# Kernel tuning notes

Measured on AMD Instinct MI355X. Metric: run time of the kernel, lower is better.

The kernel has to match this reference:

```python
import jax, jax.numpy as jnp
import numpy as np

NUM_HEADS = 16
EMB = 1024
HEAD = 64
SEQ = 2048
BATCH = 4


def setup_inputs() -> dict:
    key = jax.random.key(0)
    ks = jax.random.split(key, 6)
    s = EMB ** -0.5
    x = jax.random.normal(ks[0], (BATCH, SEQ, EMB), dtype=jnp.float32)
    # per-head projection weights stacked: [H, E, D] (Linear(emb, head, bias=False) per head)
    Wq = jax.random.normal(ks[1], (NUM_HEADS, EMB, HEAD), dtype=jnp.float32) * s
    Wk = jax.random.normal(ks[2], (NUM_HEADS, EMB, HEAD), dtype=jnp.float32) * s
    Wv = jax.random.normal(ks[3], (NUM_HEADS, EMB, HEAD), dtype=jnp.float32) * s
    # output projection Linear(head*num_heads, emb): weight [E, H*D], bias [E]
    Wo = jax.random.normal(ks[4], (EMB, NUM_HEADS * HEAD), dtype=jnp.float32) * ((NUM_HEADS * HEAD) ** -0.5)
    bo = jax.random.normal(ks[5], (EMB,), dtype=jnp.float32) * 0.01
    return {"x": x, "Wq": Wq, "Wk": Wk, "Wv": Wv, "Wo": Wo, "bo": bo}


def reference(x, Wq, Wk, Wv, Wo, bo):
    B, S, E = x.shape
    scale = HEAD ** -0.5
    # batched per-head projections: [B, H, S, D]
    q = jnp.einsum('bse,hed->bhsd', x, Wq)
    k = jnp.einsum('bse,hed->bhsd', x, Wk)
    v = jnp.einsum('bse,hed->bhsd', x, Wv)
    scores = jnp.einsum('bhqd,bhkd->bhqk', q, k) * scale
    causal = jnp.tril(jnp.ones((S, S), dtype=bool))
    scores = jnp.where(causal, scores, jnp.finfo(scores.dtype).min)
    attn = jax.nn.softmax(scores, axis=-1)  # dropout disabled (eval/deterministic)
    ctx = jnp.einsum('bhqk,bhkd->bhqd', attn, v)
    # concat heads along last dim (head-major order, matching torch.cat)
    concat = ctx.transpose(0, 2, 1, 3).reshape(B, S, NUM_HEADS * HEAD)
    out = concat @ Wo.T + bo
    return out
```

## Files before the change

### kernel.cpp

```cpp
#include <hip/hip_runtime.h>

#define NHEADS 16
#define EMB 1024
#define HDIM 64
#define SEQ 2048
#define BATCH 4

typedef unsigned short u16;
typedef __attribute__((ext_vector_type(8))) __bf16 bf16x8;
typedef __attribute__((ext_vector_type(4))) float f32x4;

#if __has_builtin(__builtin_amdgcn_exp2f)
#define EXP2(x) __builtin_amdgcn_exp2f(x)
#else
#define EXP2(x) __expf((x)*0.69314718056f)
#endif
#define CL2E 0.18033688011112042f

#define BARRIER() __builtin_amdgcn_s_barrier()
#define SB0() __builtin_amdgcn_sched_barrier(0)
#define PRIO1() __builtin_amdgcn_s_setprio(1)
#define PRIO0() __builtin_amdgcn_s_setprio(0)
#define VMCNT(n) asm volatile("s_waitcnt vmcnt(" #n ")" ::: "memory")
#define LGKM0() asm volatile("s_waitcnt lgkmcnt(0)" ::: "memory")

__device__ __forceinline__ u16 f2bf(float f) {
  union { float f; unsigned u; } v; v.f = f;
  unsigned r = v.u + 0x7fffu + ((v.u >> 16) & 1u);
  return (u16)(r >> 16);
}
__device__ __forceinline__ unsigned pk2bf(float a, float b) {
  union { __bf16 h[2]; unsigned u; } x;
  x.h[0] = (__bf16)a; x.h[1] = (__bf16)b; return x.u;
}
__device__ __forceinline__ void gl16(const void* g, void* l) {
  __builtin_amdgcn_global_load_lds(
      (const __attribute__((address_space(1))) unsigned*)g,
      (__attribute__((address_space(3))) unsigned*)l, 16, 0, 0);
}
__device__ __forceinline__ unsigned PKLO(unsigned a, unsigned b) {
  return __builtin_amdgcn_perm(a, b, 0x01000504u);
}
__device__ __forceinline__ unsigned PKHI(unsigned a, unsigned b) {
  return __builtin_amdgcn_perm(a, b, 0x03020706u);
}

__global__ __launch_bounds__(256) void k_prep(const float* __restrict__ x,
                                              const float* __restrict__ Wo,
                                              const float* __restrict__ Wq,
                                              const float* __restrict__ Wk,
                                              const float* __restrict__ Wv,
                                              u16* __restrict__ Xb,
                                              u16* __restrict__ Wob,
                                              u16* __restrict__ Wt) {
  __shared__ u16 sT[64][65];
  const int bid = blockIdx.x;
  const int t = threadIdx.x;
  if (bid < 8192) {
    int i = bid * 256 + t;
    f32x4 v = *(const f32x4*)(x + (size_t)i * 4);
    uint2 o;
    o.x = (unsigned)f2bf(v[0]) | ((unsigned)f2bf(v[1]) << 16);
    o.y = (unsigned)f2bf(v[2]) | ((unsigned)f2bf(v[3]) << 16);
    *(uint2*)(Xb + (size_t)i * 4) = o;
  } else if (bid < 9216) {
    int i = (bid - 8192) * 256 + t;
    f32x4 v = *(const f32x4*)(Wo + (size_t)i * 4);
    uint2 o;
    o.x = (unsigned)f2bf(v[0]) | ((unsigned)f2bf(v[1]) << 16);
    o.y = (unsigned)f2bf(v[2]) | ((unsigned)f2bf(v[3]) << 16);
    *(uint2*)(Wob + (size_t)i * 4) = o;
  } else {
    int pb = bid - 9216;
    const int mh = pb % 48;
    const int e0 = (pb / 48) * 64;
    const int mtx = mh >> 4, h = mh & 15;
    const float* W = (mtx == 0 ? Wq : (mtx == 1 ? Wk : Wv)) + (size_t)h * EMB * HDIM;
    {
      int e = t >> 2, d0 = (t & 3) * 16;
#pragma unroll
      for (int jj = 0; jj < 4; jj++) {
        f32x4 v = *(const f32x4*)(W + (size_t)(e0 + e) * HDIM + d0 + jj * 4);
#pragma unroll
        for (int kk = 0; kk < 4; kk++) sT[e][d0 + jj * 4 + kk] = f2bf(v[kk]);
      }
    }
    __syncthreads();
    {
      int d = t >> 2, eb = (t & 3) * 16;
#pragma unroll
      for (int j = 0; j < 16; j++)
        Wt[(size_t)(mh * 64 + d) * EMB + e0 + eb + j] = sT[eb + j][d];
    }
  }
}

__global__ __launch_bounds__(512, 2) void k_gemm_qkv8(const u16* __restrict__ Xb,
                                                      const u16* __restrict__ Wt,
                                                      u16* __restrict__ Q,
                                                      u16* __restrict__ K,
                                                      u16* __restrict__ V) {
  extern __shared__ __align__(16) char smem[];
  const int bid = blockIdx.x;
  const int l = (bid & 7) * 64 + (bid >> 3);
  const int mt = l & 31, nt = l >> 5;
  const int m0 = mt * 256, n0 = nt * 192;

  const int t = threadIdx.x;
  const int wave = t >> 6, lane = t & 63, lr = lane & 15, lg = lane >> 4;
  const int wr = (wave >> 2) * 128;
  const int wc = (wave & 3) * 48;

  const f32x4 fz = {0.f, 0.f, 0.f, 0.f};
  f32x4 acc[8][3];
#pragma unroll
  for (int i = 0; i < 8; i++)
#pragma unroll
    for (int j = 0; j < 3; j++) acc[i][j] = fz;

  bf16x8 af[4], bfr0[3], bfr1[3];

  auto SROUND = [&](char* ldsbase, int rbase, const u16* src, int gRowBase, int kt) {
    int rs = rbase + wave * 8;
    int row = rs + (lane >> 3);
    int gc = (lane & 7) ^ (row & 7);
    gl16(src + (size_t)(gRowBase + row) * EMB + kt * 64 + gc * 8, ldsbase + rs * 128);
  };
  auto LOADA4 = [&](const char* bA, int mh, int kf) {
#pragma unroll
    for (int mf = 0; mf < 4; mf++) {
      int row = wr + mh * 64 + mf * 16 + lr;
      af[mf] = *(const bf16x8*)(bA + row * 128 + ((kf * 64 + lg * 16) ^ ((row & 7) << 4)));
    }
  };
  auto LOADB3 = [&](const char* bB, int kf, bf16x8* b3) {
#pragma unroll
    for (int nf = 0; nf < 3; nf++) {
      int row = wc + nf * 16 + lr;
      b3[nf] = *(const bf16x8*)(bB + row * 128 + ((kf * 64 + lg * 16) ^ ((row & 7) << 4)));
    }
  };

#define MFMA12(MH, BF)                                                                     \
  do {                                                                                     \
    PRIO1();                                                                               \
    _Pragma("unroll") for (int mf = 0; mf < 4; mf++)                                       \
    _Pragma("unroll") for (int nf = 0; nf < 3; nf++)                                       \
      acc[(MH)*4 + mf][nf] = __builtin_amdgcn_mfma_f32_16x16x32_bf16(                      \
          af[mf], BF[nf], acc[(MH)*4 + mf][nf], 0, 0, 0);                                  \
    PRIO0();                                                                               \
  } while (0)

  const int NT = EMB / 64;
  {
    char* nA = smem;
    char* nB = smem + 32768;
    SROUND(nB, 0, Wt, n0, 0); SROUND(nB, 64, Wt, n0, 0); SROUND(nB, 128, Wt, n0, 0);
    SROUND(nA, 0, Xb, m0, 0); SROUND(nA, 64, Xb, m0, 0);
    SROUND(nA, 128, Xb, m0, 0); SROUND(nA, 192, Xb, m0, 0);
  }
  VMCNT(0);
  BARRIER();

  for (int tt = 0; tt < NT - 1; tt++) {
    const int cb = tt & 1, nb = cb ^ 1;
    char* bA = smem + cb * 57344;
    char* bB = bA + 32768;
    char* nA = smem + nb * 57344;
    char* nB = nA + 32768;
    SROUND(nB, 0, Wt, n0, tt + 1);
    SROUND(nB, 64, Wt, n0, tt + 1);
    VMCNT(2);
    BARRIER(); SB0();
    LOADB3(bB, 0, bfr0);
    LOADA4(bA, 0, 0);
    MFMA12(0, bfr0);
    BARRIER();
    SROUND(nB, 128, Wt, n0, tt + 1);
    SROUND(nA, 0, Xb, m0, tt + 1);
    LOADA4(bA, 1, 0);
    MFMA12(1, bfr0);
    BARRIER();
    SROUND(nA, 64, Xb, m0, tt + 1);
    SROUND(nA, 128, Xb, m0, tt + 1);
    LOADB3(bB, 1, bfr1);
    LOADA4(bA, 0, 1);
    MFMA12(0, bfr1);
    BARRIER();
    SROUND(nA, 192, Xb, m0, tt + 1);
    LOADA4(bA, 1, 1);
    MFMA12(1, bfr1);
    BARRIER();
  }
  {
    char* bA = smem + ((NT - 1) & 1) * 57344;
    char* bB = bA + 32768;
    VMCNT(0);
    BARRIER(); SB0();
    LOADB3(bB, 0, bfr0);
    LOADA4(bA, 0, 0);
    MFMA12(0, bfr0);
    LOADA4(bA, 1, 0);
    MFMA12(1, bfr0);
    LOADB3(bB, 1, bfr1);
    LOADA4(bA, 0, 1);
    MFMA12(0, bfr1);
    LOADA4(bA, 1, 1);
    MFMA12(1, bfr1);
  }
#undef MFMA12

  const int b = m0 >> 11;
  const int s0 = m0 & 2047;
#pragma unroll
  for (int am = 0; am < 8; am++)
#pragma unroll
    for (int nf = 0; nf < 3; nf++)
#pragma unroll
      for (int r = 0; r < 4; r++) {
        int row = wr + am * 16 + lg * 4 + r;
        int n = n0 + wc + nf * 16 + lr;
        int mtx = n >> 10, h = (n >> 6) & 15, d = n & 63;
        u16* dst = (mtx == 0 ? Q : (mtx == 1 ? K : V));
        dst[((size_t)(b * NHEADS + h) * SEQ + s0 + row) * HDIM + d] = f2bf(acc[am][nf][r]);
      }
}

__global__ __launch_bounds__(256, 3) void k_attn(const u16* __restrict__ Q,
                                                 const u16* __restrict__ K,
                                                 const u16* __restrict__ V,
                                                 u16* __restrict__ Cc) {
  const int bh = blockIdx.x;
  const int qt = 15 - (int)blockIdx.y;
  const int b = bh >> 4, h = bh & 15;
  const int t = threadIdx.x;
  const int wq = t >> 6, lane = t & 63, lr = lane & 15, lg = lane >> 4;
  const size_t base = (size_t)bh * SEQ * HDIM;

  __shared__ __align__(16) char sK[2][64 * 128];
  __shared__ __align__(16) char sV[2][64 * 128];
  __shared__ __align__(16) char sP[128 * 128];

  const int kvb = (t & 15) * 4, db = (t >> 4) * 4;
  uint2 v0, v1, v2, v3;
  auto VLOAD = [&](int k0) {
    const u16* vp = V + base + (size_t)(k0 + kvb) * HDIM + db;
    v0 = *(const uint2*)(vp);
    v1 = *(const uint2*)(vp + HDIM);
    v2 = *(const uint2*)(vp + 2 * HDIM);
    v3 = *(const uint2*)(vp + 3 * HDIM);
  };
  auto VWRITE = [&](char* sv) {
    uint2 w0 = {PKLO(v0.x, v1.x), PKLO(v2.x, v3.x)};
    uint2 w1 = {PKHI(v0.x, v1.x), PKHI(v2.x, v3.x)};
    uint2 w2 = {PKLO(v0.y, v1.y), PKLO(v2.y, v3.y)};
    uint2 w3 = {PKHI(v0.y, v1.y), PKHI(v2.y, v3.y)};
    *(uint2*)(sv + (db + 0) * 128 + ((kvb * 2) ^ (((db + 0) & 7) << 4))) = w0;
    *(uint2*)(sv + (db + 1) * 128 + ((kvb * 2) ^ (((db + 1) & 7) << 4))) = w1;
    *(uint2*)(sv + (db + 2) * 128 + ((kvb * 2) ^ (((db + 2) & 7) << 4))) = w2;
    *(uint2*)(sv + (db + 3) * 128 + ((kvb * 2) ^ (((db + 3) & 7) << 4))) = w3;
  };
  auto KSTAGE = [&](char* sk, int k0) {
#pragma unroll
    for (int i = 0; i < 2; i++) {
      int rb = wq * 16 + i * 8;
      int row = rb + (lane >> 3);
      int gc = (lane & 7) ^ (row & 7);
      gl16(K + base + (size_t)(k0 + row) * HDIM + gc * 8, sk + rb * 128);
    }
  };

#pragma unroll
  for (int i = 0; i < 4; i++) {
    int rb = wq * 32 + i * 8;
    int row = rb + (lane >> 3);
    int gc = (lane & 7) ^ (row & 7);
    gl16(Q + base + (size_t)(qt * 128 + row) * HDIM + gc * 8, sP + rb * 128);
  }
  KSTAGE(sK[0], 0);
  VLOAD(0);
  VMCNT(0);
  VWRITE(sV[0]);
  __syncthreads();

  bf16x8 qf[2][2];
#pragma unroll
  for (int q2 = 0; q2 < 2; q2++)
#pragma unroll
    for (int kf = 0; kf < 2; kf++) {
      int row = wq * 32 + q2 * 16 + lr;
      qf[q2][kf] = *(const bf16x8*)(sP + row * 128 + ((kf * 64 + lg * 16) ^ ((row & 7) << 4)));
    }

  const f32x4 fz = {0.f, 0.f, 0.f, 0.f};
  f32x4 ot[4][2];
#pragma unroll
  for (int df = 0; df < 4; df++)
#pragma unroll
    for (int q2 = 0; q2 < 2; q2++) ot[df][q2] = fz;
  float l_[2] = {0.f, 0.f};
  const float nmc = -64.f * CL2E;

  const int nsteps = 2 * qt + 2;
  for (int step = 0; step < nsteps; step++) {
    const int k0 = step * 64;
    const int cur = step & 1, nxt = cur ^ 1;
    const bool pf = (step + 1 < nsteps);
    if (pf) {
      KSTAGE(sK[nxt], k0 + 64);
      VLOAD(k0 + 64);
    }

    f32x4 st[4][2];
#pragma unroll
    for (int kvf = 0; kvf < 4; kvf++)
#pragma unroll
      for (int q2 = 0; q2 < 2; q2++) st[kvf][q2] = fz;
#pragma unroll
    for (int kf = 0; kf < 2; kf++) {
      bf16x8 kfr[4];
#pragma unroll
      for (int kvf = 0; kvf < 4; kvf++) {
        int row = kvf * 16 + lr;
        kfr[kvf] = *(const bf16x8*)(sK[cur] + row * 128 + ((kf * 64 + lg * 16) ^ ((row & 7) << 4)));
      }
      PRIO1();
#pragma unroll
      for (int kvf = 0; kvf < 4; kvf++)
#pragma unroll
        for (int q2 = 0; q2 < 2; q2++)
          st[kvf][q2] = __builtin_amdgcn_mfma_f32_16x16x32_bf16(kfr[kvf], qf[q2][kf], st[kvf][q2], 0, 0, 0);
      PRIO0();
    }

    const bool diag = (k0 >= qt * 128);
#pragma unroll
    for (int q2 = 0; q2 < 2; q2++) {
      if (diag) {
        const int qg = qt * 128 + wq * 32 + q2 * 16 + lr;
#pragma unroll
        for (int kvf = 0; kvf < 4; kvf++)
#pragma unroll
          for (int r = 0; r < 4; r++)
            if (k0 + kvf * 16 + 4 * lg + r > qg) st[kvf][q2][r] = -3e38f;
      }
      const int prow = wq * 32 + q2 * 16 + lr;
      float rs = 0.f;
#pragma unroll
      for (int kvf = 0; kvf < 4; kvf++) {
        float p0 = EXP2(fmaf(st[kvf][q2][0], CL2E, nmc));
        float p1 = EXP2(fmaf(st[kvf][q2][1], CL2E, nmc));
        float p2 = EXP2(fmaf(st[kvf][q2][2], CL2E, nmc));
        float p3 = EXP2(fmaf(st[kvf][q2][3], CL2E, nmc));
        rs += (p0 + p1) + (p2 + p3);
        uint2 w;
        w.x = pk2bf(p0, p1);
        w.y = pk2bf(p2, p3);
        *(uint2*)(sP + prow * 128 + ((kvf * 32 + lg * 8) ^ ((prow & 7) << 4))) = w;
      }
      l_[q2] += rs;
    }

#pragma unroll
    for (int kf = 0; kf < 2; kf++) {
      bf16x8 pfg[2], vf[4];
#pragma unroll
      for (int q2 = 0; q2 < 2; q2++) {
        int row = wq * 32 + q2 * 16 + lr;
        pfg[q2] = *(const bf16x8*)(sP + row * 128 + ((kf * 64 + lg * 16) ^ ((row & 7) << 4)));
      }
#pragma unroll
      for (int df = 0; df < 4; df++) {
        int row = df * 16 + lr;
        vf[df] = *(const bf16x8*)(sV[cur] + row * 128 + ((kf * 64 + lg * 16) ^ ((row & 7) << 4)));
      }
      PRIO1();
#pragma unroll
      for (int df = 0; df < 4; df++)
#pragma unroll
        for (int q2 = 0; q2 < 2; q2++)
          ot[df][q2] = __builtin_amdgcn_mfma_f32_16x16x32_bf16(vf[df], pfg[q2], ot[df][q2], 0, 0, 0);
      PRIO0();
    }

    if (pf) {
      VMCNT(0);
      VWRITE(sV[nxt]);
      LGKM0();
      BARRIER();
    }
  }

#pragma unroll
  for (int q2 = 0; q2 < 2; q2++) {
    float l = l_[q2];
    l += __shfl_xor(l, 16);
    l += __shfl_xor(l, 32);
    float inv = 1.0f / l;
    int s = qt * 128 + wq * 32 + q2 * 16 + lr;
#pragma unroll
    for (int df = 0; df < 4; df++) {
      uint2 w;
      w.x = pk2bf(ot[df][q2][0] * inv, ot[df][q2][1] * inv);
      w.y = pk2bf(ot[df][q2][2] * inv, ot[df][q2][3] * inv);
      *(uint2*)(Cc + ((size_t)b * SEQ + s) * (NHEADS * HDIM) + h * HDIM + df * 16 + 4 * lg) = w;
    }
  }
}

__global__ __launch_bounds__(512, 2) void k_gemm_out8(const u16* __restrict__ Cc,
                                                      const u16* __restrict__ Wob,
                                                      const float* __restrict__ bo,
                                                      float* __restrict__ out) {
  extern __shared__ __align__(16) char smem[];
  const int bid = blockIdx.x;
  const int l = (bid & 7) * 32 + (bid >> 3);
  const int mt = l & 31, nt = l >> 5;
  const int m0 = mt * 256, n0 = nt * 128;

  const int t = threadIdx.x;
  const int wave = t >> 6, lane = t & 63, lr = lane & 15, lg = lane >> 4;
  const int wr = (wave >> 2) * 128;
  const int wc = (wave & 3) * 32;

  const f32x4 fz = {0.f, 0.f, 0.f, 0.f};
  f32x4 acc[8][2];
#pragma unroll
  for (int i = 0; i < 8; i++)
#pragma unroll
    for (int j = 0; j < 2; j++) acc[i][j] = fz;

  bf16x8 af[4][2], bfr[2][2];

  auto SROUND = [&](char* ldsbase, int rbase, const u16* src, int gRowBase, int kt) {
    int rs = rbase + wave * 8;
    int row = rs + (lane >> 3);
    int gc = (lane & 7) ^ (row & 7);
    gl16(src + (size_t)(gRowBase + row) * EMB + kt * 64 + gc * 8, ldsbase + rs * 128);
  };
  auto STAGE6 = [&](char* nA, char* nB, int kt) {
    SROUND(nB, 0, Wob, n0, kt); SROUND(nB, 64, Wob, n0, kt);
    SROUND(nA, 0, Cc, m0, kt); SROUND(nA, 64, Cc, m0, kt);
    SROUND(nA, 128, Cc, m0, kt); SROUND(nA, 192, Cc, m0, kt);
  };
  auto LOADA = [&](const char* bA, int mh) {
#pragma unroll
    for (int mf = 0; mf < 4; mf++)
#pragma unroll
      for (int kf = 0; kf < 2; kf++) {
        int row = wr + mh * 64 + mf * 16 + lr;
        af[mf][kf] = *(const bf16x8*)(bA + row * 128 + ((kf * 64 + lg * 16) ^ ((row & 7) << 4)));
      }
  };
  auto LOADB = [&](const char* bB) {
#pragma unroll
    for (int nf = 0; nf < 2; nf++)
#pragma unroll
      for (int kf = 0; kf < 2; kf++) {
        int row = wc + nf * 16 + lr;
        bfr[nf][kf] = *(const bf16x8*)(bB + row * 128 + ((kf * 64 + lg * 16) ^ ((row & 7) << 4)));
      }
  };

#define MFMAPH2(MH)                                                                        \
  do {                                                                                     \
    _Pragma("unroll") for (int kf = 0; kf < 2; kf++)                                       \
    _Pragma("unroll") for (int mf = 0; mf < 4; mf++)                                       \
    _Pragma("unroll") for (int nf = 0; nf < 2; nf++)                                       \
      acc[(MH)*4 + mf][nf] = __builtin_amdgcn_mfma_f32_16x16x32_bf16(                      \
          af[mf][kf], bfr[nf][kf], acc[(MH)*4 + mf][nf], 0, 0, 0);                         \
  } while (0)

  const int NT = EMB / 64;
  STAGE6(smem, smem + 32768, 0);
  VMCNT(0);
  BARRIER();

  for (int tt = 0; tt < NT - 1; tt++) {
    const int cb = tt & 1, nb = cb ^ 1;
    char* bA = smem + cb * 49152;
    char* bB = bA + 32768;
    char* nA = smem + nb * 49152;
    char* nB = nA + 32768;
    STAGE6(nA, nB, tt + 1);
    VMCNT(6);
    BARRIER(); SB0();
    LOADA(bA, 0);
    LOADB(bB);
    PRIO1(); MFMAPH2(0); PRIO0();
    LOADA(bA, 1);
    PRIO1(); MFMAPH2(1); PRIO0();
    BARRIER();
  }
  {
    char* bA = smem + ((NT - 1) & 1) * 49152;
    char* bB = bA + 32768;
    VMCNT(0);
    BARRIER(); SB0();
    LOADA(bA, 0);
    LOADB(bB);
    PRIO1(); MFMAPH2(0); PRIO0();
    LOADA(bA, 1);
    PRIO1(); MFMAPH2(1); PRIO0();
  }
#undef MFMAPH2

  float bv[2];
#pragma unroll
  for (int nf = 0; nf < 2; nf++) bv[nf] = bo[n0 + wc + nf * 16 + lr];
#pragma unroll
  for (int am = 0; am < 8; am++)
#pragma unroll
    for (int nf = 0; nf < 2; nf++)
#pragma unroll
      for (int r = 0; r < 4; r++) {
        int row = wr + am * 16 + lg * 4 + r;
        int n = n0 + wc + nf * 16 + lr;
        out[(size_t)(m0 + row) * EMB + n] = acc[am][nf][r] + bv[nf];
      }
}

extern "C" void kernel_launch(void* const* d_in, const int* in_sizes, int n_in,
                              void* d_out, int out_size, void* d_ws, size_t ws_size,
                              hipStream_t stream) {
  const float* x  = (const float*)d_in[0];
  const float* Wq = (const float*)d_in[1];
  const float* Wk = (const float*)d_in[2];
  const float* Wv = (const float*)d_in[3];
  const float* Wo = (const float*)d_in[4];
  const float* bo = (const float*)d_in[5];
  float* out = (float*)d_out;

  char* ws = (char*)d_ws;
  const size_t SZ_XB  = (size_t)8192 * 1024 * 2;
  const size_t SZ_WT  = (size_t)3072 * 1024 * 2;
  const size_t SZ_WOB = (size_t)1024 * 1024 * 2;
  const size_t SZ_QKV = (size_t)64 * 2048 * 64 * 2;
  u16* Xb  = (u16*)(ws);
  u16* Wt  = (u16*)(ws + SZ_XB);
  u16* Wob = (u16*)(ws + SZ_XB + SZ_WT);
  u16* Qb  = (u16*)(ws + SZ_XB + SZ_WT + SZ_WOB);
  u16* Kb  = (u16*)(ws + SZ_XB + SZ_WT + SZ_WOB + SZ_QKV);
  u16* Vb  = (u16*)(ws + SZ_XB + SZ_WT + SZ_WOB + 2 * SZ_QKV);
  u16* Cc  = (u16*)(ws + SZ_XB + SZ_WT + SZ_WOB + 3 * SZ_QKV);

  k_prep<<<9984, 256, 0, stream>>>(x, Wo, Wq, Wk, Wv, Xb, Wob, Wt);
  k_gemm_qkv8<<<512, 512, 114688, stream>>>(Xb, Wt, Qb, Kb, Vb);
  k_attn<<<dim3(64, 16), 256, 0, stream>>>(Qb, Kb, Vb, Cc);
  k_gemm_out8<<<256, 512, 98304, stream>>>(Cc, Wob, bo, out);
}
```

Before: 159.1 us.

## Replace pipelined 256x192 QKV GEMM with simple single-buffered 128x128 tile kernel

Swaps the eight-wave, double-buffered, interleaved-schedule QKV projection GEMM (256x192 tiles, 512 blocks) for a simpler four-wave kernel with 128x128 tiles, a single LDS buffer and plain syncthreads per K step (1536 blocks). This drops the manual load/MFMA interleaving and gets more blocks, smaller LDS use and possibly higher occupancy. In exchange, global-to-LDS loads are no longer overlapped with MFMA work, and smaller tiles reduce operand reuse.

```diff
diff --git a/kernel.cpp b/kernel.cpp
--- a/kernel.cpp
+++ b/kernel.cpp
@@ -95,134 +95,77 @@
   }
 }
 
-__global__ __launch_bounds__(512, 2) void k_gemm_qkv8(const u16* __restrict__ Xb,
-                                                      const u16* __restrict__ Wt,
-                                                      u16* __restrict__ Q,
-                                                      u16* __restrict__ K,
-                                                      u16* __restrict__ V) {
-  extern __shared__ __align__(16) char smem[];
+__global__ __launch_bounds__(256) void k_gemm_qkv(const u16* __restrict__ Xb,
+                                                  const u16* __restrict__ Wt,
+                                                  u16* __restrict__ Q,
+                                                  u16* __restrict__ K,
+                                                  u16* __restrict__ V) {
   const int bid = blockIdx.x;
-  const int l = (bid & 7) * 64 + (bid >> 3);
-  const int mt = l & 31, nt = l >> 5;
-  const int m0 = mt * 256, n0 = nt * 192;
-
+  const int l = (bid & 7) * 192 + (bid >> 3);
+  const int mt = l % 64, nt = l / 64;
+  const int m0 = mt * 128, n0 = nt * 128;
   const int t = threadIdx.x;
   const int wave = t >> 6, lane = t & 63, lr = lane & 15, lg = lane >> 4;
-  const int wr = (wave >> 2) * 128;
-  const int wc = (wave & 3) * 48;
+  const int wr = (wave >> 1) * 64, wc = (wave & 1) * 64;
+
+  __shared__ __align__(16) char sA[128 * 128];
+  __shared__ __align__(16) char sB[128 * 128];
 
   const f32x4 fz = {0.f, 0.f, 0.f, 0.f};
-  f32x4 acc[8][3];
-#pragma unroll
-  for (int i = 0; i < 8; i++)
-#pragma unroll
-    for (int j = 0; j < 3; j++) acc[i][j] = fz;
-
-  bf16x8 af[4], bfr0[3], bfr1[3];
-
-  auto SROUND = [&](char* ldsbase, int rbase, const u16* src, int gRowBase, int kt) {
-    int rs = rbase + wave * 8;
-    int row = rs + (lane >> 3);
-    int gc = (lane & 7) ^ (row & 7);
-    gl16(src + (size_t)(gRowBase + row) * EMB + kt * 64 + gc * 8, ldsbase + rs * 128);
-  };
-  auto LOADA4 = [&](const char* bA, int mh, int kf) {
-#pragma unroll
-    for (int mf = 0; mf < 4; mf++) {
-      int row = wr + mh * 64 + mf * 16 + lr;
-      af[mf] = *(const bf16x8*)(bA + row * 128 + ((kf * 64 + lg * 16) ^ ((row & 7) << 4)));
-    }
-  };
-  auto LOADB3 = [&](const char* bB, int kf, bf16x8* b3) {
-#pragma unroll
-    for (int nf = 0; nf < 3; nf++) {
-      int row = wc + nf * 16 + lr;
-      b3[nf] = *(const bf16x8*)(bB + row * 128 + ((kf * 64 + lg * 16) ^ ((row & 7) << 4)));
-    }
-  };
-
-#define MFMA12(MH, BF)                                                                     \
-  do {                                                                                     \
-    PRIO1();                                                                               \
-    _Pragma("unroll") for (int mf = 0; mf < 4; mf++)                                       \
-    _Pragma("unroll") for (int nf = 0; nf < 3; nf++)                                       \
-      acc[(MH)*4 + mf][nf] = __builtin_amdgcn_mfma_f32_16x16x32_bf16(                      \
-          af[mf], BF[nf], acc[(MH)*4 + mf][nf], 0, 0, 0);                                  \
-    PRIO0();                                                                               \
-  } while (0)
-
-  const int NT = EMB / 64;
-  {
-    char* nA = smem;
-    char* nB = smem + 32768;
-    SROUND(nB, 0, Wt, n0, 0); SROUND(nB, 64, Wt, n0, 0); SROUND(nB, 128, Wt, n0, 0);
-    SROUND(nA, 0, Xb, m0, 0); SROUND(nA, 64, Xb, m0, 0);
-    SROUND(nA, 128, Xb, m0, 0); SROUND(nA, 192, Xb, m0, 0);
-  }
-  VMCNT(0);
-  BARRIER();
-
-  for (int tt = 0; tt < NT - 1; tt++) {
-    const int cb = tt & 1, nb = cb ^ 1;
-    char* bA = smem + cb * 57344;
-    char* bB = bA + 32768;
-    char* nA = smem + nb * 57344;
-    char* nB = nA + 32768;
-    SROUND(nB, 0, Wt, n0, tt + 1);
-    SROUND(nB, 64, Wt, n0, tt + 1);
-    VMCNT(2);
-    BARRIER(); SB0();
-    LOADB3(bB, 0, bfr0);
-    LOADA4(bA, 0, 0);
-    MFMA12(0, bfr0);
-    BARRIER();
-    SROUND(nB, 128, Wt, n0, tt + 1);
-    SROUND(nA, 0, Xb, m0, tt + 1);
-    LOADA4(bA, 1, 0);
-    MFMA12(1, bfr0);
-    BARRIER();
-    SROUND(nA, 64, Xb, m0, tt + 1);
-    SROUND(nA, 128, Xb, m0, tt + 1);
-    LOADB3(bB, 1, bfr1);
-    LOADA4(bA, 0, 1);
-    MFMA12(0, bfr1);
-    BARRIER();
-    SROUND(nA, 192, Xb, m0, tt + 1);
-    LOADA4(bA, 1, 1);
-    MFMA12(1, bfr1);
-    BARRIER();
-  }
-  {
-    char* bA = smem + ((NT - 1) & 1) * 57344;
-    char* bB = bA + 32768;
-    VMCNT(0);
-    BARRIER(); SB0();
-    LOADB3(bB, 0, bfr0);
-    LOADA4(bA, 0, 0);
-    MFMA12(0, bfr0);
-    LOADA4(bA, 1, 0);
-    MFMA12(1, bfr0);
-    LOADB3(bB, 1, bfr1);
-    LOADA4(bA, 0, 1);
-    MFMA12(0, bfr1);
-    LOADA4(bA, 1, 1);
-    MFMA12(1, bfr1);
-  }
-#undef MFMA12
+  f32x4 acc[4][4];
+#pragma unroll
+  for (int i = 0; i < 4; i++)
+#pragma unroll
+    for (int j = 0; j < 4; j++) acc[i][j] = fz;
+
+  for (int k0 = 0; k0 < EMB; k0 += 64) {
+#pragma unroll
+    for (int i = 0; i < 4; i++) {
+      int rb = wave * 32 + i * 8;
+      int row = rb + (lane >> 3);
+      int gc = (lane & 7) ^ (row & 7);
+      gl16(Xb + (size_t)(m0 + row) * EMB + k0 + gc * 8, sA + rb * 128);
+      gl16(Wt + (size_t)(n0 + row) * EMB + k0 + gc * 8, sB + rb * 128);
+    }
+    __syncthreads();
+    bf16x8 af[4][2], bfr[4][2];
+#pragma unroll
+    for (int mf = 0; mf < 4; mf++)
+#pragma unroll
+      for (int kf = 0; kf < 2; kf++) {
+        int row = wr + mf * 16 + lr;
+        af[mf][kf] = *(const bf16x8*)(sA + row * 128 + ((kf * 64 + lg * 16) ^ ((row & 7) << 4)));
+      }
+#pragma unroll
+    for (int nf = 0; nf < 4; nf++)
+#pragma unroll
+      for (int kf = 0; kf < 2; kf++) {
+        int row = wc + nf * 16 + lr;
+        bfr[nf][kf] = *(const bf16x8*)(sB + row * 128 + ((kf * 64 + lg * 16) ^ ((row & 7) << 4)));
+      }
+#pragma unroll
+    for (int kf = 0; kf < 2; kf++)
+#pragma unroll
+      for (int mf = 0; mf < 4; mf++)
+#pragma unroll
+        for (int nf = 0; nf < 4; nf++)
+          acc[mf][nf] = __builtin_amdgcn_mfma_f32_16x16x32_bf16(af[mf][kf], bfr[nf][kf], acc[mf][nf], 0, 0, 0);
+    __syncthreads();
+  }
 
   const int b = m0 >> 11;
   const int s0 = m0 & 2047;
 #pragma unroll
-  for (int am = 0; am < 8; am++)
-#pragma unroll
-    for (int nf = 0; nf < 3; nf++)
+  for (int mf = 0; mf < 4; mf++)
+#pragma unroll
+    for (int nf = 0; nf < 4; nf++)
 #pragma unroll
       for (int r = 0; r < 4; r++) {
-        int row = wr + am * 16 + lg * 4 + r;
+        int row = wr + mf * 16 + lg * 4 + r;
         int n = n0 + wc + nf * 16 + lr;
         int mtx = n >> 10, h = (n >> 6) & 15, d = n & 63;
         u16* dst = (mtx == 0 ? Q : (mtx == 1 ? K : V));
-        dst[((size_t)(b * NHEADS + h) * SEQ + s0 + row) * HDIM + d] = f2bf(acc[am][nf][r]);
+        dst[((size_t)(b * NHEADS + h) * SEQ + s0 + row) * HDIM + d] = f2bf(acc[mf][nf][r]);
       }
 }
 
@@ -545,7 +488,7 @@
   u16* Cc  = (u16*)(ws + SZ_XB + SZ_WT + SZ_WOB + 3 * SZ_QKV);
 
   k_prep<<<9984, 256, 0, stream>>>(x, Wo, Wq, Wk, Wv, Xb, Wob, Wt);
-  k_gemm_qkv8<<<512, 512, 114688, stream>>>(Xb, Wt, Qb, Kb, Vb);
+  k_gemm_qkv<<<1536, 256, 0, stream>>>(Xb, Wt, Qb, Kb, Vb);
   k_attn<<<dim3(64, 16), 256, 0, stream>>>(Qb, Kb, Vb, Cc);
   k_gemm_out8<<<256, 512, 98304, stream>>>(Cc, Wob, bo, out);
 }
```

Result: slower. 171.7 us (+8.0%).
